# Kernel tuning notes

Hardware: AMD Instinct MI355X
Metric: run time of the kernel (lower is better)

Reference implementation:

```python
import jax, jax.numpy as jnp
import numpy as np
from jax import lax

H = 15  # n_hidden

def _lstm_cell(x, h, c, w_ih, w_hh, b_ih, b_hh):
    # PyTorch LSTMCell gate order: i, f, g, o
    z = x @ w_ih.T + b_ih + h @ w_hh.T + b_hh  # [B, 4H]
    i, f, g, o = jnp.split(z, 4, axis=-1)
    i = jax.nn.sigmoid(i)
    f = jax.nn.sigmoid(f)
    g = jnp.tanh(g)
    o = jax.nn.sigmoid(o)
    c_new = f * c + i * g
    h_new = o * jnp.tanh(c_new)
    return h_new, c_new


def setup_inputs() -> dict:
    key = jax.random.key(0)
    ks = jax.random.split(key, 15)
    B, T = 8192, 2048
    s = 1.0 / np.sqrt(H)  # torch LSTMCell init scale
    u = lambda k, shp: jax.random.uniform(k, shp, jnp.float32, -s, s)
    inp = {
        "input": jax.random.normal(ks[0], (B, T), jnp.float32),
        "w_ih1": u(ks[1], (4 * H, 1)),
        "w_hh1": u(ks[2], (4 * H, H)),
        "b_ih1": u(ks[3], (4 * H,)),
        "b_hh1": u(ks[4], (4 * H,)),
        "w_ih2": u(ks[5], (4 * H, H)),
        "w_hh2": u(ks[6], (4 * H, H)),
        "b_ih2": u(ks[7], (4 * H,)),
        "b_hh2": u(ks[8], (4 * H,)),
        "w_ih3": u(ks[9], (4 * H, H)),
        "w_hh3": u(ks[10], (4 * H, H)),
        "b_ih3": u(ks[11], (4 * H,)),
        "b_hh3": u(ks[12], (4 * H,)),
        "w_lin": u(ks[13], (1, H)),
        "b_lin": u(ks[14], (1,)),
        "future": 0,
    }
    return inp


def reference(input, w_ih1, w_hh1, b_ih1, b_hh1,
              w_ih2, w_hh2, b_ih2, b_hh2,
              w_ih3, w_hh3, b_ih3, b_hh3,
              w_lin, b_lin, future):
    B, T = input.shape
    dtype = input.dtype
    xs = input.T[:, :, None]  # [T, B, 1]

    def step(carry, x_t):
        h1, c1, h2, c2, h3, c3 = carry
        h1, c1 = _lstm_cell(x_t, h1, c1, w_ih1, w_hh1, b_ih1, b_hh1)
        h2, c2 = _lstm_cell(h1, h2, c2, w_ih2, w_hh2, b_ih2, b_hh2)
        h3, c3 = _lstm_cell(h2, h3, c3, w_ih3, w_hh3, b_ih3, b_hh3)
        out = h3 @ w_lin.T + b_lin  # [B, 1]
        return (h1, c1, h2, c2, h3, c3), out

    init = tuple(jnp.zeros((B, H), dtype) for _ in range(6))
    carry, outs = lax.scan(step, init, xs)  # outs: [T, B, 1]
    outputs = outs[:, :, 0].T  # [B, T]

    if future > 0:
        last = outs[-1]  # [B, 1]

        def fstep(fcarry, _):
            states, out = fcarry
            states, out = step(states, out)
            return (states, out), out

        _, fouts = lax.scan(fstep, (carry, last), None, length=future)
        outputs = jnp.concatenate([outputs, fouts[:, :, 0].T], axis=1)
    return outputs
```

## Files before the change

kernel.cpp:

```cpp
#include <hip/hip_runtime.h>
#include <cstdint>

#define TT 2048
#define NH 15

typedef _Float16 half8 __attribute__((ext_vector_type(8)));
typedef float f32x4 __attribute__((ext_vector_type(4)));
typedef int int4v __attribute__((ext_vector_type(4)));

#define EXP2(x) __builtin_amdgcn_exp2f(x)
#define RCP(x) __builtin_amdgcn_rcpf(x)
#define BPERM(addr, v) __builtin_amdgcn_ds_bpermute((addr), (v))
#define PKRTZ_I(a, b) __builtin_bit_cast(int, __builtin_amdgcn_cvt_pkrtz((a), (b)))
#define MFMA16(A, B, C) __builtin_amdgcn_mfma_f32_16x16x32_f16((A), (B), (C), 0, 0, 0)

#define GATES_RAT(d0, d1, d2, d3, cref, hout) { \
    const float ui_ = EXP2(d0); \
    const float uf_ = EXP2(d1); \
    const float sg_ = EXP2(d2); \
    const float uo_ = EXP2(d3); \
    const float a_  = 1.0f + ui_; \
    const float b_  = 1.0f + sg_; \
    const float e_  = 1.0f + uf_; \
    const float ab_ = a_ * b_; \
    const float num_ = fmaf((cref), ab_, e_ * (sg_ - 1.0f)); \
    (cref) = num_ * RCP(ab_ * e_); \
    const float sc_ = EXP2((cref) * 2.8853900817779268f); \
    (hout) = (sc_ - 1.0f) * RCP((1.0f + uo_) * (sc_ + 1.0f)); }

#define LDS_BAR() { asm volatile("s_waitcnt lgkmcnt(0)" ::: "memory"); \
                    __builtin_amdgcn_s_barrier(); }

__global__ __launch_bounds__(128) __attribute__((amdgpu_waves_per_eu(1, 1)))
void lstm3_split(const float* __restrict__ input,
                 const float* __restrict__ w_ih1, const float* __restrict__ w_hh1,
                 const float* __restrict__ b_ih1, const float* __restrict__ b_hh1,
                 const float* __restrict__ w_ih2, const float* __restrict__ w_hh2,
                 const float* __restrict__ b_ih2, const float* __restrict__ b_hh2,
                 const float* __restrict__ w_ih3, const float* __restrict__ w_hh3,
                 const float* __restrict__ b_ih3, const float* __restrict__ b_hh3,
                 const float* __restrict__ w_lin, const float* __restrict__ b_lin,
                 float* __restrict__ out)
{
    __shared__ int lds[2][2][3][64];

    const int tid = threadIdx.x;
    const int w = tid >> 6;
    const int lane = tid & 63;
    const int n = lane & 15;
    const int q = lane >> 4;
    const bool q3 = (q == 3);

    for (int k = tid; k < 2 * 2 * 3 * 64; k += 128) ((int*)lds)[k] = 0;
    __syncthreads();

    const f32x4 z4 = {0.f, 0.f, 0.f, 0.f};
    const float SC[4] = {-1.4426950408889634f, -1.4426950408889634f,
                          2.8853900817779268f, -1.4426950408889634f};

    if (w == 0) {
        half8 a1[4], a3[4];
#pragma unroll
        for (int g = 0; g < 4; ++g) {
            half8 t1 = {}, t3 = {};
#pragma unroll
            for (int j = 0; j < 8; ++j) {
                const int u = 4 * q + (j & 3);
                const bool isin = (j < 4);
                float v1 = 0.f, v3 = 0.f;
                if (n < NH) {
                    const int r = g * NH + n;
                    if (isin) {
                        v1 = (u < NH) ? w_hh1[r * NH + u] : w_ih1[r];
                        v3 = (u < NH) ? w_ih3[r * NH + u] : 0.f;
                    } else {
                        v1 = (u < NH) ? 0.f : (b_ih1[r] + b_hh1[r]);
                        v3 = (u < NH) ? w_hh3[r * NH + u] : (b_ih3[r] + b_hh3[r]);
                    }
                }
                t1[j] = (_Float16)(v1 * SC[g]); t3[j] = (_Float16)(v3 * SC[g]);
            }
            a1[g] = t1; a3[g] = t3;
        }

        float h1f[4] = {0.f, 0.f, 0.f, 0.f}, c1f[4] = {0.f, 0.f, 0.f, 0.f};
        float c3a0 = 0.f, c3a1 = 0.f;
        int pA3k = 0;
        const int b1w3 = q3 ? 0x3C000000 : 0;

        const float* xrow = input + (size_t)(blockIdx.x * 16 + n) * TT;
        float xtile = xrow[q];
        float xtile_n = xrow[4 + q];
        int xp = PKRTZ_I(0.f, xtile);
        int xp_n = PKRTZ_I(0.f, xtile_n);
        int xvp = BPERM(n * 4, xp);

#pragma unroll 1
        for (int t0 = 0; t0 < TT + 4; t0 += 4) {
#pragma unroll
            for (int ph = 0; ph < 4; ++ph) {
                const int p = (t0 + ph) & 1, pr = p ^ 1;
                const int rA2 = lds[pr][1][0][lane];
                const int rB2 = lds[pr][1][1][lane];
                const int rB3 = lds[pr][1][2][lane];
                const int xps = (ph == 3) ? xp_n : xp;
                const int xvp_n = BPERM(((ph + 1) & 3) * 64 + n * 4, xps);
                const int pA1 = PKRTZ_I(h1f[0], h1f[1]);
                const int pB1 = PKRTZ_I(h1f[2], h1f[3]);
                const int b1w1 = q3
                    ? (int)((pB1 & 0xFFFF) | (xvp & (int)0xFFFF0000))
                    : pB1;
                const int4v b1 = { pA1, b1w1, 0, b1w3 };
                const int4v b3 = { rA2, rB2, pA3k, rB3 };
                const half8 B1 = __builtin_bit_cast(half8, b1);
                const half8 B3 = __builtin_bit_cast(half8, b3);
                f32x4 D10 = MFMA16(a1[0], B1, z4);
                f32x4 D11 = MFMA16(a1[1], B1, z4);
                f32x4 D12 = MFMA16(a1[2], B1, z4);
                f32x4 D13 = MFMA16(a1[3], B1, z4);
                f32x4 D30 = MFMA16(a3[0], B3, z4);
                f32x4 D31 = MFMA16(a3[1], B3, z4);
                f32x4 D32 = MFMA16(a3[2], B3, z4);
                f32x4 D33 = MFMA16(a3[3], B3, z4);
                GATES_RAT(D10[0], D11[0], D12[0], D13[0], c1f[0], h1f[0]);
                GATES_RAT(D10[1], D11[1], D12[1], D13[1], c1f[1], h1f[1]);
                GATES_RAT(D10[2], D11[2], D12[2], D13[2], c1f[2], h1f[2]);
                GATES_RAT(D10[3], D11[3], D12[3], D13[3], c1f[3], h1f[3]);
                float h3a0, h3a1;
                GATES_RAT(D30[0], D31[0], D32[0], D33[0], c3a0, h3a0);
                GATES_RAT(D30[1], D31[1], D32[1], D33[1], c3a1, h3a1);
                const int wA1 = PKRTZ_I(h1f[0], h1f[1]);
                const int wB1 = PKRTZ_I(h1f[2], h1f[3]);
                const int wA3 = PKRTZ_I(h3a0, h3a1);
                lds[p][0][0][lane] = wA1;
                lds[p][0][1][lane] = wB1;
                lds[p][0][2][lane] = wA3;
                pA3k = wA3;
                xvp = xvp_n;
                LDS_BAR();
            }
            xtile = xtile_n; xp = xp_n;
            const int tn = t0 + 8 + q;
            xtile_n = xrow[(tn < TT) ? tn : q];
            xp_n = PKRTZ_I(0.f, xtile_n);
        }
    } else {
        half8 a2[4], a3[4];
#pragma unroll
        for (int g = 0; g < 4; ++g) {
            half8 t2 = {}, t3 = {};
#pragma unroll
            for (int j = 0; j < 8; ++j) {
                const int u = 4 * q + (j & 3);
                const bool isin = (j < 4);
                float v2 = 0.f, v3 = 0.f;
                if (n < NH) {
                    const int r = g * NH + n;
                    if (isin) {
                        v2 = (u < NH) ? w_ih2[r * NH + u] : 0.f;
                        v3 = (u < NH) ? w_ih3[r * NH + u] : 0.f;
                    } else {
                        v2 = (u < NH) ? w_hh2[r * NH + u] : (b_ih2[r] + b_hh2[r]);
                        v3 = (u < NH) ? w_hh3[r * NH + u] : (b_ih3[r] + b_hh3[r]);
                    }
                }
                t2[j] = (_Float16)(v2 * SC[g]); t3[j] = (_Float16)(v3 * SC[g]);
            }
            a2[g] = t2; a3[g] = t3;
        }
        half8 ah = {};
        if (n == 0) {
#pragma unroll
            for (int j = 4; j < 8; ++j) {
                const int u = 4 * q + (j - 4);
                ah[j] = (_Float16)((u < NH) ? w_lin[u] : b_lin[0]);
            }
        }

        float c2f[4] = {0.f, 0.f, 0.f, 0.f};
        float c3b2 = 0.f, c3b3 = 0.f;
        int pA2k = 0, pB2k = 0;
        int ov2k = 0;
        int ov3k = 0;
        float y4[4] = {0.f, 0.f, 0.f, 0.f};

        float* orow = out + (size_t)(blockIdx.x * 16 + n) * TT;

#pragma unroll 1
        for (int t0 = 0; t0 < TT + 4; t0 += 4) {
#pragma unroll
            for (int ph = 0; ph < 4; ++ph) {
                const int p = (t0 + ph) & 1, pr = p ^ 1;
                const int rA1 = lds[pr][0][0][lane];
                const int rB1 = lds[pr][0][1][lane];
                const int rA3 = lds[pr][0][2][lane];
                const int4v b2 = { rA1, rB1, pA2k, ov2k };
                const int4v b3 = { pA2k, pB2k, rA3, ov3k };
                const half8 B2 = __builtin_bit_cast(half8, b2);
                const half8 B3 = __builtin_bit_cast(half8, b3);
                f32x4 D20 = MFMA16(a2[0], B2, z4);
                f32x4 D21 = MFMA16(a2[1], B2, z4);
                f32x4 D22 = MFMA16(a2[2], B2, z4);
                f32x4 D23 = MFMA16(a2[3], B2, z4);
                f32x4 D30 = MFMA16(a3[0], B3, z4);
                f32x4 D31 = MFMA16(a3[1], B3, z4);
                f32x4 D32 = MFMA16(a3[2], B3, z4);
                f32x4 D33 = MFMA16(a3[3], B3, z4);
                f32x4 Dh  = MFMA16(ah,    B3, z4);
                float h2n0, h2n1, h2n2, h2n3;
                GATES_RAT(D20[0], D21[0], D22[0], D23[0], c2f[0], h2n0);
                GATES_RAT(D20[1], D21[1], D22[1], D23[1], c2f[1], h2n1);
                GATES_RAT(D20[2], D21[2], D22[2], D23[2], c2f[2], h2n2);
                GATES_RAT(D20[3], D21[3], D22[3], D23[3], c2f[3], h2n3);
                float h3b2, h3b3;
                GATES_RAT(D30[2], D31[2], D32[2], D33[2], c3b2, h3b2);
                GATES_RAT(D30[3], D31[3], D32[3], D33[3], c3b3, h3b3);
                y4[(ph + 1) & 3] = Dh[0];
                if (ph == 2 && t0 >= 4 && q == 0) {
                    *(f32x4*)(orow + t0 - 4) =
                        (f32x4){y4[0], y4[1], y4[2], y4[3]};
                }
                const int wA2 = PKRTZ_I(h2n0, h2n1);
                const int wB2 = PKRTZ_I(h2n2, h2n3);
                const int nv2 = q3 ? (int)((wB2 & 0xFFFF) | 0x3C000000) : wB2;
                const int g3hi = (ph >= 1 || t0 > 0) ? 0x3C000000 : 0;
                const int pk3 = PKRTZ_I(h3b2, h3b3);
                const int wB3 = q3 ? (int)((pk3 & 0xFFFF) | g3hi) : pk3;
                lds[p][1][0][lane] = wA2;
                lds[p][1][1][lane] = wB2;
                lds[p][1][2][lane] = wB3;
                pA2k = wA2; pB2k = wB2; ov2k = nv2; ov3k = wB3;
                LDS_BAR();
            }
        }
    }
}

extern "C" void kernel_launch(void* const* d_in, const int* in_sizes, int n_in,
                              void* d_out, int out_size, void* d_ws, size_t ws_size,
                              hipStream_t stream) {
    const float* input = (const float*)d_in[0];
    const float* w_ih1 = (const float*)d_in[1];
    const float* w_hh1 = (const float*)d_in[2];
    const float* b_ih1 = (const float*)d_in[3];
    const float* b_hh1 = (const float*)d_in[4];
    const float* w_ih2 = (const float*)d_in[5];
    const float* w_hh2 = (const float*)d_in[6];
    const float* b_ih2 = (const float*)d_in[7];
    const float* b_hh2 = (const float*)d_in[8];
    const float* w_ih3 = (const float*)d_in[9];
    const float* w_hh3 = (const float*)d_in[10];
    const float* b_ih3 = (const float*)d_in[11];
    const float* b_hh3 = (const float*)d_in[12];
    const float* w_lin = (const float*)d_in[13];
    const float* b_lin = (const float*)d_in[14];
    float* out = (float*)d_out;

    const int B = in_sizes[0] / TT;
    const int blocks = B / 16;

    lstm3_split<<<blocks, 128, 0, stream>>>(
        input, w_ih1, w_hh1, b_ih1, b_hh1,
        w_ih2, w_hh2, b_ih2, b_hh2,
        w_ih3, w_hh3, b_ih3, b_hh3,
        w_lin, b_lin, out);
}
```

Before: 1.117 ms.

## Split the 3-layer LSTM recurrence across four waves instead of two

Work for the three LSTM layers is repartitioned from two waves per block to four. Each wave now evaluates 12 of the 48 gate-row outputs (3 cells), with hidden states exchanged through a double-buffered LDS array, including half-word stores for single cells. The goal is to shorten the serial per-timestep critical path by cutting the exp/rcp gate work each wave does per step. The cost is redundant MFMAs (waves 1 and 2 each recompute a full layer's MFMAs to get part of its output), more LDS traffic and a barrier that now spans four waves, plus two waves per SIMD pair under the new occupancy hint.

New measurement: 1.162 ms. 4.1% more time.

```diff
diff --git a/kernel.cpp b/kernel.cpp
--- a/kernel.cpp
+++ b/kernel.cpp
@@ -13,6 +13,7 @@
 #define BPERM(addr, v) __builtin_amdgcn_ds_bpermute((addr), (v))
 #define PKRTZ_I(a, b) __builtin_bit_cast(int, __builtin_amdgcn_cvt_pkrtz((a), (b)))
 #define MFMA16(A, B, C) __builtin_amdgcn_mfma_f32_16x16x32_f16((A), (B), (C), 0, 0, 0)
+#define F16LO(x) ((short)(PKRTZ_I((x), 0.0f) & 0xFFFF))
 
 #define GATES_RAT(d0, d1, d2, d3, cref, hout) { \
     const float ui_ = EXP2(d0); \
@@ -31,18 +32,18 @@
 #define LDS_BAR() { asm volatile("s_waitcnt lgkmcnt(0)" ::: "memory"); \
                     __builtin_amdgcn_s_barrier(); }
 
-__global__ __launch_bounds__(128) __attribute__((amdgpu_waves_per_eu(1, 1)))
-void lstm3_split(const float* __restrict__ input,
-                 const float* __restrict__ w_ih1, const float* __restrict__ w_hh1,
-                 const float* __restrict__ b_ih1, const float* __restrict__ b_hh1,
-                 const float* __restrict__ w_ih2, const float* __restrict__ w_hh2,
-                 const float* __restrict__ b_ih2, const float* __restrict__ b_hh2,
-                 const float* __restrict__ w_ih3, const float* __restrict__ w_hh3,
-                 const float* __restrict__ b_ih3, const float* __restrict__ b_hh3,
-                 const float* __restrict__ w_lin, const float* __restrict__ b_lin,
-                 float* __restrict__ out)
+__global__ __launch_bounds__(256) __attribute__((amdgpu_waves_per_eu(2)))
+void lstm3_split4(const float* __restrict__ input,
+                  const float* __restrict__ w_ih1, const float* __restrict__ w_hh1,
+                  const float* __restrict__ b_ih1, const float* __restrict__ b_hh1,
+                  const float* __restrict__ w_ih2, const float* __restrict__ w_hh2,
+                  const float* __restrict__ b_ih2, const float* __restrict__ b_hh2,
+                  const float* __restrict__ w_ih3, const float* __restrict__ w_hh3,
+                  const float* __restrict__ b_ih3, const float* __restrict__ b_hh3,
+                  const float* __restrict__ w_lin, const float* __restrict__ b_lin,
+                  float* __restrict__ out)
 {
-    __shared__ int lds[2][2][3][64];
+    __shared__ int lds[2][6][64];
 
     const int tid = threadIdx.x;
     const int w = tid >> 6;
@@ -51,91 +52,84 @@
     const int q = lane >> 4;
     const bool q3 = (q == 3);
 
-    for (int k = tid; k < 2 * 2 * 3 * 64; k += 128) ((int*)lds)[k] = 0;
+    for (int k = tid; k < 2 * 6 * 64; k += 256) ((int*)lds)[k] = 0;
     __syncthreads();
 
     const f32x4 z4 = {0.f, 0.f, 0.f, 0.f};
     const float SC[4] = {-1.4426950408889634f, -1.4426950408889634f,
                           2.8853900817779268f, -1.4426950408889634f};
 
+#define BUILD_A1(a) { \
+    _Pragma("unroll") \
+    for (int g = 0; g < 4; ++g) { \
+        half8 t = {}; \
+        _Pragma("unroll") \
+        for (int j = 0; j < 8; ++j) { \
+            const int u = 4 * q + (j & 3); \
+            float v = 0.f; \
+            if (n < NH) { \
+                const int r = g * NH + n; \
+                if (j < 4) v = (u < NH) ? w_hh1[r * NH + u] : w_ih1[r]; \
+                else       v = (u < NH) ? 0.f : (b_ih1[r] + b_hh1[r]); \
+            } \
+            t[j] = (_Float16)(v * SC[g]); \
+        } \
+        (a)[g] = t; \
+    } }
+#define BUILD_AX(a, wih, whh, bih, bhh) { \
+    _Pragma("unroll") \
+    for (int g = 0; g < 4; ++g) { \
+        half8 t = {}; \
+        _Pragma("unroll") \
+        for (int j = 0; j < 8; ++j) { \
+            const int u = 4 * q + (j & 3); \
+            float v = 0.f; \
+            if (n < NH) { \
+                const int r = g * NH + n; \
+                if (j < 4) v = (u < NH) ? (wih)[r * NH + u] : 0.f; \
+                else       v = (u < NH) ? (whh)[r * NH + u] \
+                                        : ((bih)[r] + (bhh)[r]); \
+            } \
+            t[j] = (_Float16)(v * SC[g]); \
+        } \
+        (a)[g] = t; \
+    } }
+
+    const float* xrow = input + (size_t)(blockIdx.x * 16 + n) * TT;
+    float* orow = out + (size_t)(blockIdx.x * 16 + n) * TT;
+
     if (w == 0) {
-        half8 a1[4], a3[4];
-#pragma unroll
-        for (int g = 0; g < 4; ++g) {
-            half8 t1 = {}, t3 = {};
-#pragma unroll
-            for (int j = 0; j < 8; ++j) {
-                const int u = 4 * q + (j & 3);
-                const bool isin = (j < 4);
-                float v1 = 0.f, v3 = 0.f;
-                if (n < NH) {
-                    const int r = g * NH + n;
-                    if (isin) {
-                        v1 = (u < NH) ? w_hh1[r * NH + u] : w_ih1[r];
-                        v3 = (u < NH) ? w_ih3[r * NH + u] : 0.f;
-                    } else {
-                        v1 = (u < NH) ? 0.f : (b_ih1[r] + b_hh1[r]);
-                        v3 = (u < NH) ? w_hh3[r * NH + u] : (b_ih3[r] + b_hh3[r]);
-                    }
-                }
-                t1[j] = (_Float16)(v1 * SC[g]); t3[j] = (_Float16)(v3 * SC[g]);
-            }
-            a1[g] = t1; a3[g] = t3;
-        }
-
-        float h1f[4] = {0.f, 0.f, 0.f, 0.f}, c1f[4] = {0.f, 0.f, 0.f, 0.f};
-        float c3a0 = 0.f, c3a1 = 0.f;
-        int pA3k = 0;
+        half8 a1[4];
+        BUILD_A1(a1)
+        float c10 = 0.f, c11 = 0.f, c12 = 0.f;
+        int W0reg = 0;
         const int b1w3 = q3 ? 0x3C000000 : 0;
-
-        const float* xrow = input + (size_t)(blockIdx.x * 16 + n) * TT;
-        float xtile = xrow[q];
-        float xtile_n = xrow[4 + q];
-        int xp = PKRTZ_I(0.f, xtile);
-        int xp_n = PKRTZ_I(0.f, xtile_n);
+        float xtile = xrow[q], xtile_n = xrow[4 + q];
+        int xp = PKRTZ_I(0.f, xtile), xp_n = PKRTZ_I(0.f, xtile_n);
         int xvp = BPERM(n * 4, xp);
-
 #pragma unroll 1
         for (int t0 = 0; t0 < TT + 4; t0 += 4) {
 #pragma unroll
             for (int ph = 0; ph < 4; ++ph) {
                 const int p = (t0 + ph) & 1, pr = p ^ 1;
-                const int rA2 = lds[pr][1][0][lane];
-                const int rB2 = lds[pr][1][1][lane];
-                const int rB3 = lds[pr][1][2][lane];
+                const int W1 = lds[pr][1][lane];
                 const int xps = (ph == 3) ? xp_n : xp;
                 const int xvp_n = BPERM(((ph + 1) & 3) * 64 + n * 4, xps);
-                const int pA1 = PKRTZ_I(h1f[0], h1f[1]);
-                const int pB1 = PKRTZ_I(h1f[2], h1f[3]);
                 const int b1w1 = q3
-                    ? (int)((pB1 & 0xFFFF) | (xvp & (int)0xFFFF0000))
-                    : pB1;
-                const int4v b1 = { pA1, b1w1, 0, b1w3 };
-                const int4v b3 = { rA2, rB2, pA3k, rB3 };
+                    ? (int)((W1 & 0xFFFF) | (xvp & (int)0xFFFF0000)) : W1;
+                const int4v b1 = { W0reg, b1w1, 0, b1w3 };
                 const half8 B1 = __builtin_bit_cast(half8, b1);
-                const half8 B3 = __builtin_bit_cast(half8, b3);
-                f32x4 D10 = MFMA16(a1[0], B1, z4);
-                f32x4 D11 = MFMA16(a1[1], B1, z4);
-                f32x4 D12 = MFMA16(a1[2], B1, z4);
-                f32x4 D13 = MFMA16(a1[3], B1, z4);
-                f32x4 D30 = MFMA16(a3[0], B3, z4);
-                f32x4 D31 = MFMA16(a3[1], B3, z4);
-                f32x4 D32 = MFMA16(a3[2], B3, z4);
-                f32x4 D33 = MFMA16(a3[3], B3, z4);
-                GATES_RAT(D10[0], D11[0], D12[0], D13[0], c1f[0], h1f[0]);
-                GATES_RAT(D10[1], D11[1], D12[1], D13[1], c1f[1], h1f[1]);
-                GATES_RAT(D10[2], D11[2], D12[2], D13[2], c1f[2], h1f[2]);
-                GATES_RAT(D10[3], D11[3], D12[3], D13[3], c1f[3], h1f[3]);
-                float h3a0, h3a1;
-                GATES_RAT(D30[0], D31[0], D32[0], D33[0], c3a0, h3a0);
-                GATES_RAT(D30[1], D31[1], D32[1], D33[1], c3a1, h3a1);
-                const int wA1 = PKRTZ_I(h1f[0], h1f[1]);
-                const int wB1 = PKRTZ_I(h1f[2], h1f[3]);
-                const int wA3 = PKRTZ_I(h3a0, h3a1);
-                lds[p][0][0][lane] = wA1;
-                lds[p][0][1][lane] = wB1;
-                lds[p][0][2][lane] = wA3;
-                pA3k = wA3;
+                f32x4 D0 = MFMA16(a1[0], B1, z4);
+                f32x4 D1 = MFMA16(a1[1], B1, z4);
+                f32x4 D2 = MFMA16(a1[2], B1, z4);
+                f32x4 D3 = MFMA16(a1[3], B1, z4);
+                float h0, h1, h2;
+                GATES_RAT(D0[0], D1[0], D2[0], D3[0], c10, h0);
+                GATES_RAT(D0[1], D1[1], D2[1], D3[1], c11, h1);
+                GATES_RAT(D0[2], D1[2], D2[2], D3[2], c12, h2);
+                W0reg = PKRTZ_I(h0, h1);
+                lds[p][0][lane] = W0reg;
+                ((short*)&lds[p][1][lane])[0] = F16LO(h2);
                 xvp = xvp_n;
                 LDS_BAR();
             }
@@ -144,30 +138,97 @@
             xtile_n = xrow[(tn < TT) ? tn : q];
             xp_n = PKRTZ_I(0.f, xtile_n);
         }
+    } else if (w == 1) {
+        half8 a1[4], a2[4];
+        BUILD_A1(a1)
+        BUILD_AX(a2, w_ih2, w_hh2, b_ih2, b_hh2)
+        float c13 = 0.f, c20 = 0.f, c21 = 0.f;
+        int W2reg = 0;
+        const int b1w3 = q3 ? 0x3C000000 : 0;
+        float xtile = xrow[q], xtile_n = xrow[4 + q];
+        int xp = PKRTZ_I(0.f, xtile), xp_n = PKRTZ_I(0.f, xtile_n);
+        int xvp = BPERM(n * 4, xp);
+#pragma unroll 1
+        for (int t0 = 0; t0 < TT + 4; t0 += 4) {
+#pragma unroll
+            for (int ph = 0; ph < 4; ++ph) {
+                const int p = (t0 + ph) & 1, pr = p ^ 1;
+                const int W0 = lds[pr][0][lane];
+                const int W1 = lds[pr][1][lane];
+                const int W3v = lds[pr][3][lane];
+                const int xps = (ph == 3) ? xp_n : xp;
+                const int xvp_n = BPERM(((ph + 1) & 3) * 64 + n * 4, xps);
+                const int b1w1 = q3
+                    ? (int)((W1 & 0xFFFF) | (xvp & (int)0xFFFF0000)) : W1;
+                const int4v b1 = { W0, b1w1, 0, b1w3 };
+                const int4v b2 = { W0, W1, W2reg, W3v };
+                const half8 B1 = __builtin_bit_cast(half8, b1);
+                const half8 B2 = __builtin_bit_cast(half8, b2);
+                f32x4 E0 = MFMA16(a1[0], B1, z4);
+                f32x4 E1 = MFMA16(a1[1], B1, z4);
+                f32x4 E2 = MFMA16(a1[2], B1, z4);
+                f32x4 E3 = MFMA16(a1[3], B1, z4);
+                f32x4 D0 = MFMA16(a2[0], B2, z4);
+                f32x4 D1 = MFMA16(a2[1], B2, z4);
+                f32x4 D2 = MFMA16(a2[2], B2, z4);
+                f32x4 D3 = MFMA16(a2[3], B2, z4);
+                float h13, h20, h21;
+                GATES_RAT(E0[3], E1[3], E2[3], E3[3], c13, h13);
+                GATES_RAT(D0[0], D1[0], D2[0], D3[0], c20, h20);
+                GATES_RAT(D0[1], D1[1], D2[1], D3[1], c21, h21);
+                ((short*)&lds[p][1][lane])[1] = F16LO(h13);
+                W2reg = PKRTZ_I(h20, h21);
+                lds[p][2][lane] = W2reg;
+                xvp = xvp_n;
+                LDS_BAR();
+            }
+            xtile = xtile_n; xp = xp_n;
+            const int tn = t0 + 8 + q;
+            xtile_n = xrow[(tn < TT) ? tn : q];
+            xp_n = PKRTZ_I(0.f, xtile_n);
+        }
+    } else if (w == 2) {
+        half8 a2[4], a3[4];
+        BUILD_AX(a2, w_ih2, w_hh2, b_ih2, b_hh2)
+        BUILD_AX(a3, w_ih3, w_hh3, b_ih3, b_hh3)
+        float c22 = 0.f, c23 = 0.f, c30 = 0.f;
+        int W3vreg = 0;
+#pragma unroll 1
+        for (int t0 = 0; t0 < TT + 4; t0 += 4) {
+#pragma unroll
+            for (int ph = 0; ph < 4; ++ph) {
+                const int p = (t0 + ph) & 1, pr = p ^ 1;
+                const int W0 = lds[pr][0][lane];
+                const int W1 = lds[pr][1][lane];
+                const int W2 = lds[pr][2][lane];
+                const int W4 = lds[pr][4][lane];
+                const int W5v = lds[pr][5][lane];
+                const int4v b2 = { W0, W1, W2, W3vreg };
+                const int4v b3 = { W2, W3vreg, W4, W5v };
+                const half8 B2 = __builtin_bit_cast(half8, b2);
+                const half8 B3 = __builtin_bit_cast(half8, b3);
+                f32x4 D0 = MFMA16(a2[0], B2, z4);
+                f32x4 D1 = MFMA16(a2[1], B2, z4);
+                f32x4 D2 = MFMA16(a2[2], B2, z4);
+                f32x4 D3 = MFMA16(a2[3], B2, z4);
+                f32x4 E0 = MFMA16(a3[0], B3, z4);
+                f32x4 E1 = MFMA16(a3[1], B3, z4);
+                f32x4 E2 = MFMA16(a3[2], B3, z4);
+                f32x4 E3 = MFMA16(a3[3], B3, z4);
+                float h22, h23, h30;
+                GATES_RAT(D0[2], D1[2], D2[2], D3[2], c22, h22);
+                GATES_RAT(D0[3], D1[3], D2[3], D3[3], c23, h23);
+                GATES_RAT(E0[0], E1[0], E2[0], E3[0], c30, h30);
+                const int pk2 = PKRTZ_I(h22, h23);
+                W3vreg = q3 ? (int)((pk2 & 0xFFFF) | 0x3C000000) : pk2;
+                lds[p][3][lane] = W3vreg;
+                ((short*)&lds[p][4][lane])[0] = F16LO(h30);
+                LDS_BAR();
+            }
+        }
     } else {
-        half8 a2[4], a3[4];
-#pragma unroll
-        for (int g = 0; g < 4; ++g) {
-            half8 t2 = {}, t3 = {};
-#pragma unroll
-            for (int j = 0; j < 8; ++j) {
-                const int u = 4 * q + (j & 3);
-                const bool isin = (j < 4);
-                float v2 = 0.f, v3 = 0.f;
-                if (n < NH) {
-                    const int r = g * NH + n;
-                    if (isin) {
-                        v2 = (u < NH) ? w_ih2[r * NH + u] : 0.f;
-                        v3 = (u < NH) ? w_ih3[r * NH + u] : 0.f;
-                    } else {
-                        v2 = (u < NH) ? w_hh2[r * NH + u] : (b_ih2[r] + b_hh2[r]);
-                        v3 = (u < NH) ? w_hh3[r * NH + u] : (b_ih3[r] + b_hh3[r]);
-                    }
-                }
-                t2[j] = (_Float16)(v2 * SC[g]); t3[j] = (_Float16)(v3 * SC[g]);
-            }
-            a2[g] = t2; a3[g] = t3;
-        }
+        half8 a3[4];
+        BUILD_AX(a3, w_ih3, w_hh3, b_ih3, b_hh3)
         half8 ah = {};
         if (n == 0) {
 #pragma unroll
@@ -176,64 +237,44 @@
                 ah[j] = (_Float16)((u < NH) ? w_lin[u] : b_lin[0]);
             }
         }
-
-        float c2f[4] = {0.f, 0.f, 0.f, 0.f};
-        float c3b2 = 0.f, c3b3 = 0.f;
-        int pA2k = 0, pB2k = 0;
-        int ov2k = 0;
-        int ov3k = 0;
+        float c31 = 0.f, c32 = 0.f, c33 = 0.f;
+        int W5vreg = 0;
         float y4[4] = {0.f, 0.f, 0.f, 0.f};
-
-        float* orow = out + (size_t)(blockIdx.x * 16 + n) * TT;
-
 #pragma unroll 1
         for (int t0 = 0; t0 < TT + 4; t0 += 4) {
 #pragma unroll
             for (int ph = 0; ph < 4; ++ph) {
                 const int p = (t0 + ph) & 1, pr = p ^ 1;
-                const int rA1 = lds[pr][0][0][lane];
-                const int rB1 = lds[pr][0][1][lane];
-                const int rA3 = lds[pr][0][2][lane];
-                const int4v b2 = { rA1, rB1, pA2k, ov2k };
-                const int4v b3 = { pA2k, pB2k, rA3, ov3k };
-                const half8 B2 = __builtin_bit_cast(half8, b2);
+                const int W2 = lds[pr][2][lane];
+                const int W3v = lds[pr][3][lane];
+                const int W4 = lds[pr][4][lane];
+                const int4v b3 = { W2, W3v, W4, W5vreg };
                 const half8 B3 = __builtin_bit_cast(half8, b3);
-                f32x4 D20 = MFMA16(a2[0], B2, z4);
-                f32x4 D21 = MFMA16(a2[1], B2, z4);
-                f32x4 D22 = MFMA16(a2[2], B2, z4);
-                f32x4 D23 = MFMA16(a2[3], B2, z4);
-                f32x4 D30 = MFMA16(a3[0], B3, z4);
-                f32x4 D31 = MFMA16(a3[1], B3, z4);
-                f32x4 D32 = MFMA16(a3[2], B3, z4);
-                f32x4 D33 = MFMA16(a3[3], B3, z4);
-                f32x4 Dh  = MFMA16(ah,    B3, z4);
-                float h2n0, h2n1, h2n2, h2n3;
-                GATES_RAT(D20[0], D21[0], D22[0], D23[0], c2f[0], h2n0);
-                GATES_RAT(D20[1], D21[1], D22[1], D23[1], c2f[1], h2n1);
-                GATES_RAT(D20[2], D21[2], D22[2], D23[2], c2f[2], h2n2);
-                GATES_RAT(D20[3], D21[3], D22[3], D23[3], c2f[3], h2n3);
-                float h3b2, h3b3;
-                GATES_RAT(D30[2], D31[2], D32[2], D33[2], c3b2, h3b2);
-                GATES_RAT(D30[3], D31[3], D32[3], D33[3], c3b3, h3b3);
+                f32x4 E0 = MFMA16(a3[0], B3, z4);
+                f32x4 E1 = MFMA16(a3[1], B3, z4);
+                f32x4 E2 = MFMA16(a3[2], B3, z4);
+                f32x4 E3 = MFMA16(a3[3], B3, z4);
+                f32x4 Dh = MFMA16(ah, B3, z4);
+                float h31, h32, h33;
+                GATES_RAT(E0[1], E1[1], E2[1], E3[1], c31, h31);
+                GATES_RAT(E0[2], E1[2], E2[2], E3[2], c32, h32);
+                GATES_RAT(E0[3], E1[3], E2[3], E3[3], c33, h33);
                 y4[(ph + 1) & 3] = Dh[0];
                 if (ph == 2 && t0 >= 4 && q == 0) {
                     *(f32x4*)(orow + t0 - 4) =
                         (f32x4){y4[0], y4[1], y4[2], y4[3]};
                 }
-                const int wA2 = PKRTZ_I(h2n0, h2n1);
-                const int wB2 = PKRTZ_I(h2n2, h2n3);
-                const int nv2 = q3 ? (int)((wB2 & 0xFFFF) | 0x3C000000) : wB2;
+                ((short*)&lds[p][4][lane])[1] = F16LO(h31);
+                const int pk3 = PKRTZ_I(h32, h33);
                 const int g3hi = (ph >= 1 || t0 > 0) ? 0x3C000000 : 0;
-                const int pk3 = PKRTZ_I(h3b2, h3b3);
-                const int wB3 = q3 ? (int)((pk3 & 0xFFFF) | g3hi) : pk3;
-                lds[p][1][0][lane] = wA2;
-                lds[p][1][1][lane] = wB2;
-                lds[p][1][2][lane] = wB3;
-                pA2k = wA2; pB2k = wB2; ov2k = nv2; ov3k = wB3;
+                W5vreg = q3 ? (int)((pk3 & 0xFFFF) | g3hi) : pk3;
+                lds[p][5][lane] = W5vreg;
                 LDS_BAR();
             }
         }
     }
+#undef BUILD_A1
+#undef BUILD_AX
 }
 
 extern "C" void kernel_launch(void* const* d_in, const int* in_sizes, int n_in,
@@ -259,7 +300,7 @@
     const int B = in_sizes[0] / TT;
     const int blocks = B / 16;
 
-    lstm3_split<<<blocks, 128, 0, stream>>>(
+    lstm3_split4<<<blocks, 256, 0, stream>>>(
         input, w_ih1, w_hh1, b_ih1, b_hh1,
         w_ih2, w_hh2, b_ih2, b_hh2,
         w_ih3, w_hh3, b_ih3, b_hh3,
```
